# Performance work log

Measured on AMD Instinct MI355X. Metric: run time of the kernel, lower is better.

## Reference

```python
import jax, jax.numpy as jnp
import numpy as np

B, S, D, M = 16, 2048, 1024, 256


def setup_inputs() -> dict:
    key = jax.random.key(0)
    ks = jax.random.split(key, 5)
    w_scale = 0.03  # ~xavier for these fan sizes
    return {
        "x": jax.random.normal(ks[0], (B, S, D), jnp.float32),
        "Wi": jax.random.normal(ks[1], (M, D), jnp.float32) * w_scale,
        "bi": jnp.zeros((M,), jnp.float32),
        "Wf": jax.random.normal(ks[2], (M, D + M), jnp.float32) * w_scale,
        "bf": jnp.ones((M,), jnp.float32),  # forget bias init = 1.0
        "Wu": jax.random.normal(ks[3], (M, D + M), jnp.float32) * w_scale,
        "bu": jnp.zeros((M,), jnp.float32),
        "Wo": jax.random.normal(ks[4], (D, D + M), jnp.float32) * w_scale,
        "bo": jnp.zeros((D,), jnp.float32),
    }


def reference(x, Wi, bi, Wf, bf, Wu, bu, Wo, bo):
    # x: [B, S, D]; gate weights [out, D+M] split into x-part and h-part.
    d = x.shape[-1]
    m = Wi.shape[0]
    WfH, WuH, WoH = Wf[:, d:], Wu[:, d:], Wo[:, d:]
    # Precompute all input-dependent projections (parallel over time).
    xm = jax.nn.silu(jnp.einsum('bsd,md->bsm', x, Wi) + bi)          # SiLU(memory_proj_in(x_t))
    xf = jnp.einsum('bsd,md->bsm', x, Wf[:, :d]) + bf                # x-part of forget gate
    xu = jnp.einsum('bsd,md->bsm', x, Wu[:, :d]) + bu                # x-part of update gate
    xo = x + jnp.einsum('bsd,od->bso', x, Wo[:, :d]) + bo            # residual + x-part of output gate

    def step(h, ts):
        xf_t, xu_t, xm_t, xo_t = ts
        f = jax.nn.sigmoid(xf_t + h @ WfH.T)
        u = jax.nn.sigmoid(xu_t + h @ WuH.T)
        h_new = f * h + u * xm_t            # dropout is identity in eval mode
        out = xo_t + h_new @ WoH.T
        return h_new, out

    h0 = jnp.zeros((x.shape[0], m), x.dtype)
    xs = (xf.swapaxes(0, 1), xu.swapaxes(0, 1), xm.swapaxes(0, 1), xo.swapaxes(0, 1))
    h_final, outs = jax.lax.scan(step, h0, xs)   # outs: [S, B, D]
    return outs.swapaxes(0, 1), h_final
```

## Files before the change

kernel.cpp:

```cpp
#include <hip/hip_runtime.h>
#include <cstdint>
#include <cstddef>

typedef __attribute__((ext_vector_type(8))) short short8;
typedef __attribute__((ext_vector_type(4))) short short4v;
typedef __attribute__((ext_vector_type(4))) float float4v;

typedef __attribute__((address_space(3))) uint32_t lds_u32;
typedef const __attribute__((address_space(1))) uint32_t gl_u32;

__device__ __forceinline__ short f2bf(float f) {
    union { float f; uint32_t u; } v; v.f = f;
    uint32_t r = v.u + 0x7fffu + ((v.u >> 16) & 1u);
    return (short)(r >> 16);
}
__device__ __forceinline__ float bf2f(short s) {
    union { uint32_t u; float f; } v; v.u = ((uint32_t)(uint16_t)s) << 16;
    return v.f;
}
__device__ __forceinline__ float sigmoidf_(float z) {
    return 1.0f / (1.0f + __expf(-z));
}

__global__ __launch_bounds__(256) void xconvert_kernel(const float* __restrict__ x,
                                                       short* __restrict__ Xcat) {
    size_t i = ((size_t)blockIdx.x * 256 + threadIdx.x) * 4;
    size_t r = i >> 10, c = i & 1023;
    float4v v = *(const float4v*)(x + i);
    short4v o;
#pragma unroll
    for (int j = 0; j < 4; ++j) o[j] = f2bf(v[j]);
    *(short4v*)(Xcat + r * 1280 + c) = o;
}

__global__ __launch_bounds__(256) void wconvert_kernel(const float* __restrict__ Wi,
                                                       const float* __restrict__ Wf,
                                                       const float* __restrict__ Wu,
                                                       const float* __restrict__ Wo,
                                                       short* __restrict__ W3b,
                                                       short* __restrict__ Wob) {
    int i = blockIdx.x * 256 + threadIdx.x;
    if (i < 768 * 1024) {
        int n = i >> 10, k = i & 1023;
        const float* src = (n < 256) ? (Wi + (size_t)n * 1024 + k)
                         : (n < 512) ? (Wf + (size_t)(n - 256) * 1280 + k)
                                     : (Wu + (size_t)(n - 512) * 1280 + k);
        W3b[i] = f2bf(*src);
    } else {
        int j = i - 768 * 1024;
        Wob[j] = f2bf(Wo[j]);
    }
}

template <int EPI>
__global__ __launch_bounds__(256) void gemm_bt(const short* __restrict__ A,
                                               const short* __restrict__ Bmat,
                                               const int K, const int lda,
                                               const float* __restrict__ bias1,
                                               const float* __restrict__ bias2,
                                               const float* __restrict__ bias3,
                                               const float* __restrict__ xres,
                                               float* __restrict__ outf,
                                               short* __restrict__ outb) {
    __shared__ __align__(16) short As[4096];
    __shared__ __align__(16) short Bs[4096];

    const int tid = threadIdx.x;
    const int lane = tid & 63;
    const int wv = tid >> 6;
    const int wm = wv >> 1, wn = wv & 1;
    const int row15 = lane & 15;
    const int q = lane >> 4;
    const int tileM = blockIdx.x * 128;
    const int tileN = blockIdx.y * 128;

    float4v acc[4][4];
#pragma unroll
    for (int i = 0; i < 4; ++i)
#pragma unroll
        for (int j = 0; j < 4; ++j) acc[i][j] = {0.f, 0.f, 0.f, 0.f};

    const short* aG = A + (size_t)(tileM + (tid >> 2)) * lda + (tid & 3) * 8;
    const short* bG = Bmat + (size_t)(tileN + (tid >> 2)) * K + (tid & 3) * 8;
    const size_t aStep = (size_t)64 * lda;
    const size_t bStep = (size_t)64 * K;

    lds_u32* AsL = (lds_u32*)As;
    lds_u32* BsL = (lds_u32*)Bs;
    const int base1 = wv * 256;
    const int base2 = 1024 + wv * 256;

    for (int kt = 0; kt < K; kt += 32) {
        __builtin_amdgcn_global_load_lds((gl_u32*)aG,           AsL + base1, 16, 0, 0);
        __builtin_amdgcn_global_load_lds((gl_u32*)(aG + aStep), AsL + base2, 16, 0, 0);
        __builtin_amdgcn_global_load_lds((gl_u32*)bG,           BsL + base1, 16, 0, 0);
        __builtin_amdgcn_global_load_lds((gl_u32*)(bG + bStep), BsL + base2, 16, 0, 0);
        aG += 32; bG += 32;
        __syncthreads();

        short8 af[4], bf8[4];
#pragma unroll
        for (int mt = 0; mt < 4; ++mt)
            af[mt] = *(const short8*)(As + (wm * 64 + mt * 16 + row15) * 32 + q * 8);
#pragma unroll
        for (int nt = 0; nt < 4; ++nt)
            bf8[nt] = *(const short8*)(Bs + (wn * 64 + nt * 16 + row15) * 32 + q * 8);
#pragma unroll
        for (int mt = 0; mt < 4; ++mt)
#pragma unroll
            for (int nt = 0; nt < 4; ++nt)
                acc[mt][nt] = __builtin_amdgcn_mfma_f32_16x16x32_bf16(af[mt], bf8[nt], acc[mt][nt], 0, 0, 0);
        __syncthreads();
    }

#pragma unroll
    for (int mt = 0; mt < 4; ++mt) {
#pragma unroll
        for (int nt = 0; nt < 4; ++nt) {
#pragma unroll
            for (int r = 0; r < 4; ++r) {
                const int gr = tileM + wm * 64 + mt * 16 + q * 4 + r;
                const int gc = tileN + wn * 64 + nt * 16 + row15;
                float v = acc[mt][nt][r];
                if (EPI == 1) {
                    float bias = (gc < 256) ? bias1[gc] : (gc < 512) ? bias2[gc - 256] : bias3[gc - 512];
                    float z = v + bias;
                    if (gc < 256) z = z * sigmoidf_(z);
                    outb[(size_t)gr * 768 + gc] = f2bf(z);
                } else {
                    const size_t idx = (size_t)gr * 1024 + gc;
                    outf[idx] = v + bias1[gc] + xres[idx];
                }
            }
        }
    }
}

__global__ __launch_bounds__(512, 2) void scan_kernel(const float* __restrict__ Wfp,
                                                      const float* __restrict__ Wup,
                                                      const short* __restrict__ xmfu,
                                                      short* __restrict__ Xcat,
                                                      float* __restrict__ hfinal) {
    __shared__ __align__(16) short hb[2][256];
    __shared__ __align__(16) short xstage[2][6144];

    const int tid = threadIdx.x;
    const int lane = tid & 63;
    const int w = tid >> 6;
    const int n0 = w * 32;
    const int row15 = lane & 15;
    const int q = lane >> 4;
    const int b = blockIdx.x;

    const short* xm_b = xmfu + (size_t)b * 1572864;

    ((short*)hb)[tid] = 0;

    short8 bfrag[8][2][2];
#pragma unroll
    for (int ks = 0; ks < 8; ++ks)
#pragma unroll
        for (int sel = 0; sel < 2; ++sel)
#pragma unroll
            for (int nt = 0; nt < 2; ++nt) {
                const float* WH = sel ? Wup : Wfp;
                const float* src = WH + (size_t)(n0 + nt * 16 + row15) * 1280 + 1024 + ks * 32 + q * 8;
                float4v v0 = *(const float4v*)(src);
                float4v v1 = *(const float4v*)(src + 4);
                short8 v;
#pragma unroll
                for (int j = 0; j < 4; ++j) { v[j] = f2bf(v0[j]); v[j + 4] = f2bf(v1[j]); }
                bfrag[ks][sel][nt] = v;
            }

    const bool isLoader = (tid >= 256);
    const int lw = (tid - 256) >> 6;
    lds_u32* xl = (lds_u32*)(&xstage[0][0]);

    if (isLoader) {
#pragma unroll
        for (int i = 0; i < 3; ++i)
            __builtin_amdgcn_global_load_lds((gl_u32*)(xm_b + i * 2048 + lw * 512 + lane * 8),
                                             xl + (i * 1024 + lw * 256), 16, 0, 0);
        __builtin_amdgcn_sched_barrier(0);
        asm volatile("s_waitcnt vmcnt(0)" ::: "memory");
        __builtin_amdgcn_sched_barrier(0);
    }
    __builtin_amdgcn_sched_barrier(0);
    asm volatile("s_waitcnt lgkmcnt(0)" ::: "memory");
    __builtin_amdgcn_sched_barrier(0);
    __builtin_amdgcn_s_barrier();
    __builtin_amdgcn_sched_barrier(0);

    float h1 = 0.f, h2 = 0.f;
    const int m1 = n0 + row15;
    short* Xout1 = Xcat + (size_t)b * 2048 * 1280 + 1024 + m1;
    short* Xout2 = Xout1 + 16;

    short8 afr = {0, 0, 0, 0, 0, 0, 0, 0};

#pragma unroll 1
    for (int j = 0; j < 256; ++j) {
        const int buf = j & 1;
        if (isLoader && (j + 1 < 256)) {
            const short* src = xm_b + (size_t)(j + 1) * 6144;
#pragma unroll
            for (int i = 0; i < 3; ++i)
                __builtin_amdgcn_global_load_lds((gl_u32*)(src + i * 2048 + lw * 512 + lane * 8),
                                                 xl + ((buf ^ 1) * 3072 + i * 1024 + lw * 256), 16, 0, 0);
        }
        const short* xs = &xstage[buf][0];
#pragma unroll
        for (int s = 0; s < 8; ++s) {
            const int p = s & 1;
            float xmv1, xmv2, zf1, zf2, zu1, zu2;
            if (lane < 16) {
                xmv1 = bf2f(xs[s * 768 + m1]);
                zf1  = bf2f(xs[s * 768 + 256 + m1]);
                zu1  = bf2f(xs[s * 768 + 512 + m1]);
                xmv2 = bf2f(xs[s * 768 + 16 + m1]);
                zf2  = bf2f(xs[s * 768 + 272 + m1]);
                zu2  = bf2f(xs[s * 768 + 528 + m1]);
            }
            float4v af0 = {0.f, 0.f, 0.f, 0.f}, af1 = {0.f, 0.f, 0.f, 0.f};
            float4v au0 = {0.f, 0.f, 0.f, 0.f}, au1 = {0.f, 0.f, 0.f, 0.f};
#pragma unroll
            for (int ks = 0; ks < 8; ++ks) {
                if (row15 == 0)
                    afr = *(const short8*)(&hb[p][ks * 32 + q * 8]);
                af0 = __builtin_amdgcn_mfma_f32_16x16x32_bf16(afr, bfrag[ks][0][0], af0, 0, 0, 0);
                af1 = __builtin_amdgcn_mfma_f32_16x16x32_bf16(afr, bfrag[ks][0][1], af1, 0, 0, 0);
                au0 = __builtin_amdgcn_mfma_f32_16x16x32_bf16(afr, bfrag[ks][1][0], au0, 0, 0, 0);
                au1 = __builtin_amdgcn_mfma_f32_16x16x32_bf16(afr, bfrag[ks][1][1], au1, 0, 0, 0);
            }
            if (lane < 16) {
                const float f1 = sigmoidf_(af0[0] + zf1);
                const float u1 = sigmoidf_(au0[0] + zu1);
                const float f2 = sigmoidf_(af1[0] + zf2);
                const float u2 = sigmoidf_(au1[0] + zu2);
                h1 = f1 * h1 + u1 * xmv1;
                h2 = f2 * h2 + u2 * xmv2;
                const short s1 = f2bf(h1), s2 = f2bf(h2);
                hb[p ^ 1][m1] = s1;
                hb[p ^ 1][m1 + 16] = s2;
                const size_t off = (size_t)(j * 8 + s) * 1280;
                Xout1[off] = s1;
                Xout2[off] = s2;
            }
            if (s == 7 && isLoader) {
                __builtin_amdgcn_sched_barrier(0);
                asm volatile("s_waitcnt vmcnt(0)" ::: "memory");
                __builtin_amdgcn_sched_barrier(0);
            }
            __builtin_amdgcn_sched_barrier(0);
            asm volatile("s_waitcnt lgkmcnt(0)" ::: "memory");
            __builtin_amdgcn_sched_barrier(0);
            __builtin_amdgcn_s_barrier();
            __builtin_amdgcn_sched_barrier(0);
        }
    }
    if (lane < 16) {
        hfinal[b * 256 + m1] = h1;
        hfinal[b * 256 + m1 + 16] = h2;
    }
}

extern "C" void kernel_launch(void* const* d_in, const int* in_sizes, int n_in,
                              void* d_out, int out_size, void* d_ws, size_t ws_size,
                              hipStream_t stream) {
    const float* x  = (const float*)d_in[0];
    const float* Wi = (const float*)d_in[1];
    const float* bi = (const float*)d_in[2];
    const float* Wf = (const float*)d_in[3];
    const float* bf = (const float*)d_in[4];
    const float* Wu = (const float*)d_in[5];
    const float* bu = (const float*)d_in[6];
    const float* Wo = (const float*)d_in[7];
    const float* bo = (const float*)d_in[8];
    float* out = (float*)d_out;

    char* ws = (char*)d_ws;
    short* Xcat = (short*)ws;
    short* xmfu = (short*)(ws + 83886080ULL);
    short* W3b  = (short*)(ws + 83886080ULL + 50331648ULL);
    short* Wob  = (short*)(ws + 83886080ULL + 50331648ULL + 1572864ULL);

    xconvert_kernel<<<dim3(32768), dim3(256), 0, stream>>>(x, Xcat);
    wconvert_kernel<<<dim3(8192), dim3(256), 0, stream>>>(Wi, Wf, Wu, Wo, W3b, Wob);
    gemm_bt<1><<<dim3(256, 6), dim3(256), 0, stream>>>(Xcat, W3b, 1024, 1280,
                                                       bi, bf, bu, nullptr, nullptr, xmfu);
    scan_kernel<<<dim3(16), dim3(512), 0, stream>>>(Wf, Wu, xmfu, Xcat, out + 33554432);
    gemm_bt<2><<<dim3(256, 8), dim3(256), 0, stream>>>(Xcat, Wob, 1280, 1280,
                                                       bo, nullptr, nullptr, x, out, nullptr);
}
```

Measured before the change: 2.417 ms.

## Buffer hidden-state history in LDS and write it out with coalesced vector stores

The scan kernel now keeps eight timesteps of h in a double-buffered LDS history instead of two ping-pong rows. Copier waves write the previous chunk to the output with 16-byte coalesced stores, replacing the scattered 2-byte per-step global stores in the serial critical path. It also splits the MFMA accumulation into two independent chains to shorten dependency latency, and raises wave priority around the MFMA block. Loader duty moves to waves 0-3 and copying to waves 4-7, which adds a small amount of LDS use.

```diff
diff --git a/kernel.cpp b/kernel.cpp
--- a/kernel.cpp
+++ b/kernel.cpp
@@ -141,7 +141,7 @@
                                                       const short* __restrict__ xmfu,
                                                       short* __restrict__ Xcat,
                                                       float* __restrict__ hfinal) {
-    __shared__ __align__(16) short hb[2][256];
+    __shared__ __align__(16) short hist[2][8][256];
     __shared__ __align__(16) short xstage[2][6144];
 
     const int tid = threadIdx.x;
@@ -153,8 +153,9 @@
     const int b = blockIdx.x;
 
     const short* xm_b = xmfu + (size_t)b * 1572864;
-
-    ((short*)hb)[tid] = 0;
+    short* XoutBase = Xcat + (size_t)b * 2048 * 1280 + 1024;
+
+    for (int i = tid; i < 4096; i += 512) ((short*)hist)[i] = 0;
 
     short8 bfrag[8][2][2];
 #pragma unroll
@@ -173,15 +174,15 @@
                 bfrag[ks][sel][nt] = v;
             }
 
-    const bool isLoader = (tid >= 256);
-    const int lw = (tid - 256) >> 6;
     lds_u32* xl = (lds_u32*)(&xstage[0][0]);
+    const bool isLoader = (w < 4);
+    const bool isCopier = (w >= 4);
 
     if (isLoader) {
 #pragma unroll
         for (int i = 0; i < 3; ++i)
-            __builtin_amdgcn_global_load_lds((gl_u32*)(xm_b + i * 2048 + lw * 512 + lane * 8),
-                                             xl + (i * 1024 + lw * 256), 16, 0, 0);
+            __builtin_amdgcn_global_load_lds((gl_u32*)(xm_b + i * 2048 + w * 512 + lane * 8),
+                                             xl + (i * 1024 + w * 256), 16, 0, 0);
         __builtin_amdgcn_sched_barrier(0);
         asm volatile("s_waitcnt vmcnt(0)" ::: "memory");
         __builtin_amdgcn_sched_barrier(0);
@@ -194,26 +195,30 @@
 
     float h1 = 0.f, h2 = 0.f;
     const int m1 = n0 + row15;
-    short* Xout1 = Xcat + (size_t)b * 2048 * 1280 + 1024 + m1;
-    short* Xout2 = Xout1 + 16;
+
+    const int s0r = 2 * (w - 4) + (lane >> 5);
+    const int cOff = (lane & 31) * 8;
 
     short8 afr = {0, 0, 0, 0, 0, 0, 0, 0};
 
 #pragma unroll 1
     for (int j = 0; j < 256; ++j) {
-        const int buf = j & 1;
+        const int jb = j & 1;
         if (isLoader && (j + 1 < 256)) {
             const short* src = xm_b + (size_t)(j + 1) * 6144;
 #pragma unroll
             for (int i = 0; i < 3; ++i)
-                __builtin_amdgcn_global_load_lds((gl_u32*)(src + i * 2048 + lw * 512 + lane * 8),
-                                                 xl + ((buf ^ 1) * 3072 + i * 1024 + lw * 256), 16, 0, 0);
+                __builtin_amdgcn_global_load_lds((gl_u32*)(src + i * 2048 + w * 512 + lane * 8),
+                                                 xl + ((jb ^ 1) * 3072 + i * 1024 + w * 256), 16, 0, 0);
         }
-        const short* xs = &xstage[buf][0];
+        if (isCopier && j >= 1) {
+            short8 hv = *(const short8*)(&hist[jb ^ 1][s0r][cOff]);
+            *(short8*)(XoutBase + (size_t)(8 * (j - 1) + s0r) * 1280 + cOff) = hv;
+        }
+        const short* xs = &xstage[jb][0];
 #pragma unroll
         for (int s = 0; s < 8; ++s) {
-            const int p = s & 1;
-            float xmv1, xmv2, zf1, zf2, zu1, zu2;
+            float xmv1 = 0.f, xmv2 = 0.f, zf1 = 0.f, zf2 = 0.f, zu1 = 0.f, zu2 = 0.f;
             if (lane < 16) {
                 xmv1 = bf2f(xs[s * 768 + m1]);
                 zf1  = bf2f(xs[s * 768 + 256 + m1]);
@@ -222,30 +227,38 @@
                 zf2  = bf2f(xs[s * 768 + 272 + m1]);
                 zu2  = bf2f(xs[s * 768 + 528 + m1]);
             }
-            float4v af0 = {0.f, 0.f, 0.f, 0.f}, af1 = {0.f, 0.f, 0.f, 0.f};
-            float4v au0 = {0.f, 0.f, 0.f, 0.f}, au1 = {0.f, 0.f, 0.f, 0.f};
+            const short* hprev = (s == 0) ? &hist[jb ^ 1][7][0] : &hist[jb][s - 1][0];
+
+            float4v acc[2][2][2];
+#pragma unroll
+            for (int sel = 0; sel < 2; ++sel)
+#pragma unroll
+                for (int nt = 0; nt < 2; ++nt)
+#pragma unroll
+                    for (int hf = 0; hf < 2; ++hf) acc[sel][nt][hf] = {0.f, 0.f, 0.f, 0.f};
+
+            __builtin_amdgcn_s_setprio(1);
 #pragma unroll
             for (int ks = 0; ks < 8; ++ks) {
                 if (row15 == 0)
-                    afr = *(const short8*)(&hb[p][ks * 32 + q * 8]);
-                af0 = __builtin_amdgcn_mfma_f32_16x16x32_bf16(afr, bfrag[ks][0][0], af0, 0, 0, 0);
-                af1 = __builtin_amdgcn_mfma_f32_16x16x32_bf16(afr, bfrag[ks][0][1], af1, 0, 0, 0);
-                au0 = __builtin_amdgcn_mfma_f32_16x16x32_bf16(afr, bfrag[ks][1][0], au0, 0, 0, 0);
-                au1 = __builtin_amdgcn_mfma_f32_16x16x32_bf16(afr, bfrag[ks][1][1], au1, 0, 0, 0);
-            }
+                    afr = *(const short8*)(hprev + ks * 32 + q * 8);
+                const int hf = ks & 1;
+                acc[0][0][hf] = __builtin_amdgcn_mfma_f32_16x16x32_bf16(afr, bfrag[ks][0][0], acc[0][0][hf], 0, 0, 0);
+                acc[0][1][hf] = __builtin_amdgcn_mfma_f32_16x16x32_bf16(afr, bfrag[ks][0][1], acc[0][1][hf], 0, 0, 0);
+                acc[1][0][hf] = __builtin_amdgcn_mfma_f32_16x16x32_bf16(afr, bfrag[ks][1][0], acc[1][0][hf], 0, 0, 0);
+                acc[1][1][hf] = __builtin_amdgcn_mfma_f32_16x16x32_bf16(afr, bfrag[ks][1][1], acc[1][1][hf], 0, 0, 0);
+            }
+            __builtin_amdgcn_s_setprio(0);
+
             if (lane < 16) {
-                const float f1 = sigmoidf_(af0[0] + zf1);
-                const float u1 = sigmoidf_(au0[0] + zu1);
-                const float f2 = sigmoidf_(af1[0] + zf2);
-                const float u2 = sigmoidf_(au1[0] + zu2);
+                const float f1 = sigmoidf_(acc[0][0][0][0] + acc[0][0][1][0] + zf1);
+                const float u1 = sigmoidf_(acc[1][0][0][0] + acc[1][0][1][0] + zu1);
+                const float f2 = sigmoidf_(acc[0][1][0][0] + acc[0][1][1][0] + zf2);
+                const float u2 = sigmoidf_(acc[1][1][0][0] + acc[1][1][1][0] + zu2);
                 h1 = f1 * h1 + u1 * xmv1;
                 h2 = f2 * h2 + u2 * xmv2;
-                const short s1 = f2bf(h1), s2 = f2bf(h2);
-                hb[p ^ 1][m1] = s1;
-                hb[p ^ 1][m1 + 16] = s2;
-                const size_t off = (size_t)(j * 8 + s) * 1280;
-                Xout1[off] = s1;
-                Xout2[off] = s2;
+                hist[jb][s][m1] = f2bf(h1);
+                hist[jb][s][m1 + 16] = f2bf(h2);
             }
             if (s == 7 && isLoader) {
                 __builtin_amdgcn_sched_barrier(0);
@@ -258,6 +271,10 @@
             __builtin_amdgcn_s_barrier();
             __builtin_amdgcn_sched_barrier(0);
         }
+    }
+    if (isCopier) {
+        short8 hv = *(const short8*)(&hist[1][s0r][cOff]);
+        *(short8*)(XoutBase + (size_t)(2040 + s0r) * 1280 + cOff) = hv;
     }
     if (lane < 16) {
         hfinal[b * 256 + m1] = h1;
```

New measurement: 2.404 ms. About the same (-0.5%).
